# Performance work log

Hardware: AMD Instinct MI355X
Metric: run time of the kernel (lower is better)

The kernel has to match this reference:

```python
import jax, jax.numpy as jnp
import numpy as np

TEMP = 0.1
LAM = 1.0
NORM_EPS = 1e-12   # torch F.normalize eps
COS_EPS = 1e-8     # torch F.cosine_similarity eps


def l2norm(x, axis):
    n = jnp.sqrt(jnp.sum(x * x, axis=axis, keepdims=True))
    return x / jnp.maximum(n, NORM_EPS)


def cos_sim(a, b, axis):
    na = jnp.sqrt(jnp.sum(a * a, axis=axis))
    nb = jnp.sqrt(jnp.sum(b * b, axis=axis))
    return jnp.sum(a * b, axis=axis) / jnp.maximum(na * nb, COS_EPS)


def setup_inputs() -> dict:
    key = jax.random.key(0)
    k1, k2, k3, k4, k5 = jax.random.split(key, 5)
    B, C, H, W = 32, 256, 32, 32
    return {
        "q_b": jax.random.normal(k1, (B, C, H, W), dtype=jnp.float32),
        "k_b": jax.random.normal(k2, (B, C, H, W), dtype=jnp.float32),
        "q_grid": jax.random.normal(k3, (B, C, H, W), dtype=jnp.float32),
        "k_grid": jax.random.normal(k4, (B, C, H, W), dtype=jnp.float32),
        "labels": jax.random.randint(k5, (B,), 0, 10, dtype=jnp.int64),
    }


def densecl(q_b, k_b, q_grid, k_grid, labels):
    B, C, H, W = q_b.shape
    S = H * W
    q_b = l2norm(q_b, axis=1)
    k_b = l2norm(k_b, axis=1)
    q_grid = l2norm(q_grid, axis=1)
    k_grid = l2norm(k_grid, axis=1)

    q_b_flat = q_b.reshape(B, C, S)
    k_b_flat = k_b.reshape(B, C, S)
    # spatial correspondence: [B, S, S]
    sim = jnp.einsum('bci,bcj->bij', q_b_flat, k_b_flat)
    max_sim_idx = jnp.argmax(sim, axis=-1)  # [B, S]

    Cg = q_grid.shape[1]
    q_grid_flat = q_grid.reshape(B, Cg, S)
    k_grid_flat = k_grid.reshape(B, Cg, S)
    idx = jnp.broadcast_to(max_sim_idx[:, None, :], (B, Cg, S))
    k_matched = jnp.take_along_axis(k_grid_flat, idx, axis=2)
    pos_sim = cos_sim(q_grid_flat, k_matched, axis=1) / TEMP  # [B, S]

    # random negative from a different-label sample (use_prototypes=False path)
    key = jax.random.key(42)
    u = jax.random.uniform(key, (B, B))
    mask = labels[:, None] != labels[None, :]
    neg_idx = jnp.argmax(jnp.where(mask, u, -1.0), axis=1)  # [B]
    neg_k = k_grid_flat[neg_idx]  # [B, Cg, S]
    neg_sim = cos_sim(q_grid_flat, neg_k, axis=1) / TEMP  # [B, S]

    loss = -jnp.log(jnp.exp(pos_sim) / (jnp.exp(pos_sim) + jnp.exp(neg_sim) + 1e-6))
    return jnp.mean(loss)


def reference(q_b, k_b, q_grid, k_grid, labels):
    return densecl(q_b, k_b, q_grid, k_grid, labels) * LAM
```

## Files before the change

kernel.cpp:

```cpp
#include <hip/hip_runtime.h>
#include <hip/hip_bf16.h>
#include <math.h>
#include <stdint.h>

#define BB 32
#define CC 256
#define SS 1024

typedef __attribute__((ext_vector_type(8))) short short8v;
typedef __attribute__((ext_vector_type(4))) float f32x4;

#define ASYNC16(g, l)                                                        \
  __builtin_amdgcn_global_load_lds(                                          \
      (const __attribute__((address_space(1))) void*)(g),                    \
      (__attribute__((address_space(3))) void*)(l), 16, 0, 0)

__device__ __forceinline__ unsigned short bf16_rne(float f) {
  unsigned int u = __float_as_uint(f);
  unsigned int r = (u + 0x7fffu + ((u >> 16) & 1u)) >> 16;
  return (unsigned short)r;
}

__global__ __launch_bounds__(256, 4) void transnorm_kernel(
    const float* __restrict__ srcA, const float* __restrict__ srcB,
    unsigned short* __restrict__ dstA, unsigned short* __restrict__ dstB,
    float* __restrict__ invA, float* __restrict__ invB) {
  const int bid = blockIdx.x;
  const int which = bid >> 10;
  const int sub = bid & 1023;
  const int b = sub >> 5;
  const int s0 = (sub & 31) * 32;

  const float* src = which ? srcB : srcA;
  unsigned short* dst = which ? dstB : dstA;
  float* inv = which ? invB : invA;

  __shared__ float st[256][33];
  __shared__ float part[8][33];

  const int tid = threadIdx.x;
  const int s_l = tid & 31, c_off = tid >> 5;

  const float* sp = src + (size_t)b * CC * SS + s0 + s_l;
  float ssq = 0.f;
#pragma unroll 8
  for (int p = 0; p < 32; ++p) {
    int c = p * 8 + c_off;
    float x = sp[(size_t)c << 10];
    ssq = fmaf(x, x, ssq);
    st[c][s_l] = x;
  }
  part[c_off][s_l] = ssq;
  __syncthreads();

  const int chunk = tid >> 3, rb8 = tid & 7;
  unsigned short* dp = dst + ((size_t)b * SS + s0) * CC;
#pragma unroll
  for (int r0 = 0; r0 < 32; r0 += 8) {
    int r = r0 + rb8;
    unsigned short u[8];
#pragma unroll
    for (int uu = 0; uu < 8; ++uu) u[uu] = bf16_rne(st[chunk * 8 + uu][r]);
    uint4 pk;
    pk.x = (unsigned)u[0] | ((unsigned)u[1] << 16);
    pk.y = (unsigned)u[2] | ((unsigned)u[3] << 16);
    pk.z = (unsigned)u[4] | ((unsigned)u[5] << 16);
    pk.w = (unsigned)u[6] | ((unsigned)u[7] << 16);
    *(uint4*)(dp + (size_t)r * CC + chunk * 8) = pk;
  }
  if (inv != nullptr && tid < 32) {
    float s = 0.f;
#pragma unroll
    for (int k = 0; k < 8; ++k) s += part[k][tid];
    inv[b * SS + s0 + tid] = 1.0f / fmaxf(sqrtf(s), 1e-12f);
  }
}

__global__ __launch_bounds__(256, 4) void simargmax_mfma(
    const unsigned short* __restrict__ qt, const unsigned short* __restrict__ kt,
    const float* __restrict__ invk, unsigned long long* __restrict__ best) {
  const int i_raw = blockIdx.x;
  const int xcd = i_raw & 7;
  const int u = i_raw >> 3;
  const int b = ((u >> 6) << 3) | xcd;
  const int tile = u & 63;
  const int it = tile >> 3, jt = tile & 7;
  const int t = threadIdx.x, w = t >> 6, l = t & 63;

  __shared__ unsigned short sa[128 * 64];
  __shared__ unsigned short sb[128 * 64];
  __shared__ unsigned long long cand2[128][2];
  __shared__ float sinvk[128];

  if (t < 128) sinvk[t] = invk[b * SS + jt * 128 + t];

  const unsigned short* aG = qt + ((size_t)b * SS + it * 128) * CC;
  const unsigned short* bG = kt + ((size_t)b * SS + jt * 128) * CC;

  f32x4 acc[4][4];
#pragma unroll
  for (int mt = 0; mt < 4; ++mt)
#pragma unroll
    for (int nt = 0; nt < 4; ++nt) acc[mt][nt] = (f32x4){0.f, 0.f, 0.f, 0.f};

  const int r8 = l >> 3, p = l & 7;
  const int q4 = l >> 4, m16 = l & 15;
  const int wi = (w >> 1) * 64, wj = (w & 1) * 64;

  for (int ch = 0; ch < 4; ++ch) {
    __syncthreads();
#pragma unroll
    for (int v = 0; v < 4; ++v) {
      int r = v * 32 + w * 8 + r8;
      int clog = p ^ (r & 7);
      ASYNC16(aG + (size_t)r * CC + ch * 64 + clog * 8, &sa[(v * 32 + w * 8) * 64]);
      ASYNC16(bG + (size_t)r * CC + ch * 64 + clog * 8, &sb[(v * 32 + w * 8) * 64]);
    }
    __syncthreads();
#pragma unroll
    for (int kk = 0; kk < 2; ++kk) {
      short8v af[4], bf[4];
#pragma unroll
      for (int mt = 0; mt < 4; ++mt) {
        int i = wi + mt * 16 + m16;
        int cp = (kk * 4 + q4) ^ (i & 7);
        af[mt] = *(const short8v*)&sa[i * 64 + cp * 8];
        int j = wj + mt * 16 + m16;
        int cq = (kk * 4 + q4) ^ (j & 7);
        bf[mt] = *(const short8v*)&sb[j * 64 + cq * 8];
      }
#pragma unroll
      for (int mt = 0; mt < 4; ++mt)
#pragma unroll
        for (int nt = 0; nt < 4; ++nt)
          acc[mt][nt] = __builtin_amdgcn_mfma_f32_16x16x32_bf16(
              af[mt], bf[nt], acc[mt][nt], 0, 0, 0);
    }
  }

  float siv[4];
#pragma unroll
  for (int nt = 0; nt < 4; ++nt) siv[nt] = sinvk[wj + nt * 16 + m16];

#pragma unroll
  for (int mt = 0; mt < 4; ++mt) {
    unsigned long long bp[4];
#pragma unroll
    for (int e = 0; e < 4; ++e) {
      unsigned long long mx = 0ull;
#pragma unroll
      for (int nt = 0; nt < 4; ++nt) {
        float v = acc[mt][nt][e] * siv[nt];
        unsigned int uu = __float_as_uint(v);
        uu = (uu & 0x80000000u) ? ~uu : (uu | 0x80000000u);
        int col = jt * 128 + wj + nt * 16 + m16;
        unsigned long long pk =
            ((unsigned long long)uu << 32) | (unsigned)(1023 - col);
        mx = (pk > mx) ? pk : mx;
      }
      bp[e] = mx;
    }
#pragma unroll
    for (int d = 1; d < 16; d <<= 1) {
#pragma unroll
      for (int e = 0; e < 4; ++e) {
        unsigned long long o = __shfl_xor(bp[e], d, 64);
        if (o > bp[e]) bp[e] = o;
      }
    }
    if (m16 == 0) {
#pragma unroll
      for (int e = 0; e < 4; ++e)
        cand2[wi + mt * 16 + q4 * 4 + e][w & 1] = bp[e];
    }
  }
  __syncthreads();
  if (t < 128) {
    unsigned long long m0 = cand2[t][0], m1 = cand2[t][1];
    atomicMax(&best[b * SS + it * 128 + t], m0 > m1 ? m0 : m1);
  }
}

__device__ __forceinline__ void tf_round(uint32_t& x0, uint32_t& x1, int r) {
  x0 += x1;
  x1 = (x1 << r) | (x1 >> (32 - r));
  x1 ^= x0;
}

__global__ void negidx_kernel(const int* __restrict__ labels, int* __restrict__ negidx) {
  __shared__ float u[1024];
  int t = threadIdx.x;
  uint32_t x0 = (uint32_t)t;
  uint32_t x1 = (uint32_t)(t + 512);
  const uint32_t ks0 = 0u, ks1 = 42u, ks2 = 0x1BD11BDAu ^ 0u ^ 42u;
  x0 += ks0; x1 += ks1;
  tf_round(x0, x1, 13); tf_round(x0, x1, 15); tf_round(x0, x1, 26); tf_round(x0, x1, 6);
  x0 += ks1; x1 += ks2 + 1u;
  tf_round(x0, x1, 17); tf_round(x0, x1, 29); tf_round(x0, x1, 16); tf_round(x0, x1, 24);
  x0 += ks2; x1 += ks0 + 2u;
  tf_round(x0, x1, 13); tf_round(x0, x1, 15); tf_round(x0, x1, 26); tf_round(x0, x1, 6);
  x0 += ks0; x1 += ks1 + 3u;
  tf_round(x0, x1, 17); tf_round(x0, x1, 29); tf_round(x0, x1, 16); tf_round(x0, x1, 24);
  x0 += ks1; x1 += ks2 + 4u;
  tf_round(x0, x1, 13); tf_round(x0, x1, 15); tf_round(x0, x1, 26); tf_round(x0, x1, 6);
  x0 += ks2; x1 += ks0 + 5u;
  u[t]       = __uint_as_float((x0 >> 9) | 0x3f800000u) - 1.0f;
  u[t + 512] = __uint_as_float((x1 >> 9) | 0x3f800000u) - 1.0f;
  __syncthreads();
  if (t < BB) {
    int lb = labels[t];
    float bestv = -1.0f;
    int bj = 0;
    for (int j = 0; j < BB; ++j) {
      float v = (labels[j] != lb) ? u[t * BB + j] : -1.0f;
      if (v > bestv) { bestv = v; bj = j; }
    }
    negidx[t] = bj;
  }
}

__global__ __launch_bounds__(256) void loss_fused_kernel(
    const float* __restrict__ qg, const unsigned short* __restrict__ kgt,
    const float* __restrict__ invkg, const unsigned long long* __restrict__ best,
    const int* __restrict__ negidx, float* __restrict__ out) {
  const int tid = threadIdx.x;
  const int s_l = tid & 31, g = tid >> 5;
  const int P0 = blockIdx.x * 32;
  const int b = P0 >> 10;
  const int s = (P0 & (SS - 1)) + s_l;
  const int idx = b * SS + s;
  const int js = 1023 - (int)(best[idx] & 0xffffffffu);
  const int nb = negidx[b];

  const float* qcol = qg + ((size_t)b * CC + g * 32) * SS + s;
  const unsigned short* kp = kgt + ((size_t)b * SS + js) * CC + g * 32;
  const unsigned short* kn = kgt + ((size_t)nb * SS + s) * CC + g * 32;

  float dp = 0.f, dn = 0.f, sq = 0.f;
#pragma unroll
  for (int uu = 0; uu < 4; ++uu) {
    uint4 up = *(const uint4*)(kp + uu * 8);
    uint4 un = *(const uint4*)(kn + uu * 8);
    float q[8];
#pragma unroll
    for (int j = 0; j < 8; ++j) {
      q[j] = qcol[(size_t)(uu * 8 + j) << 10];
      sq = fmaf(q[j], q[j], sq);
    }
    float pv[8], nv[8];
    pv[0] = __uint_as_float(up.x << 16); pv[1] = __uint_as_float(up.x & 0xffff0000u);
    pv[2] = __uint_as_float(up.y << 16); pv[3] = __uint_as_float(up.y & 0xffff0000u);
    pv[4] = __uint_as_float(up.z << 16); pv[5] = __uint_as_float(up.z & 0xffff0000u);
    pv[6] = __uint_as_float(up.w << 16); pv[7] = __uint_as_float(up.w & 0xffff0000u);
    nv[0] = __uint_as_float(un.x << 16); nv[1] = __uint_as_float(un.x & 0xffff0000u);
    nv[2] = __uint_as_float(un.y << 16); nv[3] = __uint_as_float(un.y & 0xffff0000u);
    nv[4] = __uint_as_float(un.z << 16); nv[5] = __uint_as_float(un.z & 0xffff0000u);
    nv[6] = __uint_as_float(un.w << 16); nv[7] = __uint_as_float(un.w & 0xffff0000u);
#pragma unroll
    for (int j = 0; j < 8; ++j) {
      dp = fmaf(q[j], pv[j], dp);
      dn = fmaf(q[j], nv[j], dn);
    }
  }

  __shared__ float rdp[8][33], rdn[8][33], rsq[8][33];
  rdp[g][s_l] = dp;
  rdn[g][s_l] = dn;
  rsq[g][s_l] = sq;
  __syncthreads();
  if (tid < 32) {
    float DP = 0.f, DN = 0.f, SQ = 0.f;
#pragma unroll
    for (int k = 0; k < 8; ++k) {
      DP += rdp[k][tid];
      DN += rdn[k][tid];
      SQ += rsq[k][tid];
    }
    int s2 = (P0 & (SS - 1)) + tid;
    int idx2 = b * SS + s2;
    int js2 = 1023 - (int)(best[idx2] & 0xffffffffu);
    float iq = 1.0f / fmaxf(sqrtf(SQ), 1e-12f);
    float pvv = DP * iq * invkg[b * SS + js2] * 10.0f;
    float nvv = DN * iq * invkg[nb * SS + s2] * 10.0f;
    float elem = logf(expf(pvv) + expf(nvv) + 1e-6f) - pvv;
#pragma unroll
    for (int o = 16; o > 0; o >>= 1) elem += __shfl_down(elem, o, 32);
    if (tid == 0) atomicAdd(out, elem * (1.0f / (BB * SS)));
  }
}

__global__ __launch_bounds__(256) void norms_kernel(
    const float* __restrict__ qb, const float* __restrict__ kb,
    const float* __restrict__ qg, const float* __restrict__ kg,
    float* __restrict__ inv) {
  int t = blockIdx.x * 256 + threadIdx.x;
  int which = t >> 15;
  int bs = t & (BB * SS - 1);
  const float* src = (which == 0) ? qb : (which == 1) ? kb : (which == 2) ? qg : kg;
  int b = bs >> 10;
  int s = bs & (SS - 1);
  const float* p = src + (size_t)b * CC * SS + s;
  float ss = 0.f;
#pragma unroll 8
  for (int c = 0; c < CC; ++c) {
    float x = p[(size_t)c * SS];
    ss = fmaf(x, x, ss);
  }
  float n = fmaxf(sqrtf(ss), 1e-12f);
  inv[t] = 1.0f / n;
}

#define TI 64
#define TJ 128
#define KC 32

__global__ __launch_bounds__(256) void simargmax_kernel(
    const float* __restrict__ qb, const float* __restrict__ kb,
    const float* __restrict__ invq, const float* __restrict__ invk,
    int* __restrict__ amax) {
  const int b = blockIdx.x >> 4;
  const int i0 = (blockIdx.x & 15) * TI;
  const int t = threadIdx.x;
  const int ti = t >> 4;
  const int tj = t & 15;

  __shared__ float aQ[KC][TI];
  __shared__ float bK[KC][TJ];
  __shared__ float redv[TI][16];
  __shared__ int redj[TI][16];

  const float* qbase = qb + (size_t)b * CC * SS + i0;
  const float* kbase = kb + (size_t)b * CC * SS;
  const float* ivq = invq + b * SS + i0;
  const float* ivk = invk + b * SS;

  float best_v = -3.4e38f;
  int best_j = 0;

  for (int j0 = 0; j0 < SS; j0 += TJ) {
    float acc[4][8];
#pragma unroll
    for (int r = 0; r < 4; ++r)
#pragma unroll
      for (int rr = 0; rr < 8; ++rr) acc[r][rr] = 0.f;

    for (int c0 = 0; c0 < CC; c0 += KC) {
      __syncthreads();
#pragma unroll
      for (int v = 0; v < 2; ++v) {
        int f = t + v * 256;
        int cl = f >> 4;
        int sl = (f & 15) << 2;
        float4 qa = *(const float4*)(qbase + (size_t)(c0 + cl) * SS + sl);
        float4 iv = *(const float4*)(ivq + sl);
        aQ[cl][sl + 0] = qa.x * iv.x;
        aQ[cl][sl + 1] = qa.y * iv.y;
        aQ[cl][sl + 2] = qa.z * iv.z;
        aQ[cl][sl + 3] = qa.w * iv.w;
      }
#pragma unroll
      for (int v = 0; v < 4; ++v) {
        int f = t + v * 256;
        int cl = f >> 5;
        int sl = (f & 31) << 2;
        float4 ka = *(const float4*)(kbase + (size_t)(c0 + cl) * SS + j0 + sl);
        float4 ik = *(const float4*)(ivk + j0 + sl);
        bK[cl][sl + 0] = ka.x * ik.x;
        bK[cl][sl + 1] = ka.y * ik.y;
        bK[cl][sl + 2] = ka.z * ik.z;
        bK[cl][sl + 3] = ka.w * ik.w;
      }
      __syncthreads();
#pragma unroll
      for (int kc = 0; kc < KC; ++kc) {
        float4 a0 = *(const float4*)&aQ[kc][ti * 4];
        float4 b0 = *(const float4*)&bK[kc][tj * 8];
        float4 b1 = *(const float4*)&bK[kc][tj * 8 + 4];
        float av[4] = {a0.x, a0.y, a0.z, a0.w};
        float bv[8] = {b0.x, b0.y, b0.z, b0.w, b1.x, b1.y, b1.z, b1.w};
#pragma unroll
        for (int r = 0; r < 4; ++r)
#pragma unroll
          for (int rr = 0; rr < 8; ++rr)
            acc[r][rr] = fmaf(av[r], bv[rr], acc[r][rr]);
      }
    }
    __syncthreads();
#pragma unroll
    for (int r = 0; r < 4; ++r) {
      float v = acc[r][0];
      int jb = j0 + tj * 8;
#pragma unroll
      for (int rr = 1; rr < 8; ++rr) {
        if (acc[r][rr] > v) { v = acc[r][rr]; jb = j0 + tj * 8 + rr; }
      }
      redv[ti * 4 + r][tj] = v;
      redj[ti * 4 + r][tj] = jb;
    }
    __syncthreads();
    if (t < TI) {
#pragma unroll
      for (int ww = 0; ww < 16; ++ww) {
        float v = redv[t][ww];
        if (v > best_v) { best_v = v; best_j = redj[t][ww]; }
      }
    }
  }
  if (t < TI) amax[b * SS + i0 + t] = best_j;
}

__global__ __launch_bounds__(256) void loss_kernel(
    const float* __restrict__ qg, const float* __restrict__ kg,
    const float* __restrict__ invq, const float* __restrict__ invk,
    const int* __restrict__ amax, const int* __restrict__ negidx,
    float* __restrict__ out) {
  int t = blockIdx.x * 256 + threadIdx.x;
  int b = t >> 10;
  int s = t & (SS - 1);
  int js = amax[t];
  int nb = negidx[b];
  const float* qcol = qg + (size_t)b * CC * SS + s;
  const float* kpcol = kg + (size_t)b * CC * SS + js;
  const float* kncol = kg + (size_t)nb * CC * SS + s;
  float dp = 0.f, dn = 0.f;
#pragma unroll 8
  for (int c = 0; c < CC; ++c) {
    float q = qcol[(size_t)c * SS];
    dp = fmaf(q, kpcol[(size_t)c * SS], dp);
    dn = fmaf(q, kncol[(size_t)c * SS], dn);
  }
  float iq = invq[t];
  float pv = dp * iq * invk[b * SS + js] * 10.0f;
  float nv = dn * iq * invk[nb * SS + s] * 10.0f;
  float elem = logf(expf(pv) + expf(nv) + 1e-6f) - pv;

  __shared__ float red[256];
  red[threadIdx.x] = elem;
  __syncthreads();
  for (int o = 128; o > 0; o >>= 1) {
    if (threadIdx.x < o) red[threadIdx.x] += red[threadIdx.x + o];
    __syncthreads();
  }
  if (threadIdx.x == 0) atomicAdd(out, red[0] * (1.0f / (BB * SS)));
}

extern "C" void kernel_launch(void* const* d_in, const int* in_sizes, int n_in,
                              void* d_out, int out_size, void* d_ws, size_t ws_size,
                              hipStream_t stream) {
  const float* qb = (const float*)d_in[0];
  const float* kb = (const float*)d_in[1];
  const float* qg = (const float*)d_in[2];
  const float* kg = (const float*)d_in[3];
  const int* labels = (const int*)d_in[4];

  char* ws = (char*)d_ws;
  float* invkb = (float*)ws;
  float* invkg = (float*)(ws + 128 * 1024);
  unsigned long long* best = (unsigned long long*)(ws + 256 * 1024);
  int* negidx = (int*)(ws + 512 * 1024);
  unsigned short* qt = (unsigned short*)(ws + (1 << 20));
  unsigned short* kt = (unsigned short*)(ws + (17 << 20));
  unsigned short* kgt = (unsigned short*)(ws + (33 << 20));

  const size_t need = (size_t)50 * 1024 * 1024;
  const bool fast = ws_size >= need;

  hipMemsetAsync(d_out, 0, sizeof(float), stream);

  if (fast) {
    hipMemsetAsync(best, 0, BB * SS * sizeof(unsigned long long), stream);
    negidx_kernel<<<1, 512, 0, stream>>>(labels, negidx);
    transnorm_kernel<<<2048, 256, 0, stream>>>(qb, kb, qt, kt, nullptr, invkb);
    simargmax_mfma<<<2048, 256, 0, stream>>>(qt, kt, invkb, best);
    transnorm_kernel<<<1024, 256, 0, stream>>>(kg, kg, kgt, kgt, invkg, invkg);
    loss_fused_kernel<<<1024, 256, 0, stream>>>(qg, kgt, invkg, best, negidx,
                                                (float*)d_out);
  } else {
    float* inv = (float*)ws;
    int* amax = (int*)(ws + 512 * 1024);
    int* negidx2 = (int*)(ws + 640 * 1024);
    norms_kernel<<<(4 * BB * SS) / 256, 256, 0, stream>>>(qb, kb, qg, kg, inv);
    simargmax_kernel<<<BB * (SS / TI), 256, 0, stream>>>(
        qb, kb, inv + 0 * BB * SS, inv + 1 * BB * SS, amax);
    negidx_kernel<<<1, 512, 0, stream>>>(labels, negidx2);
    loss_kernel<<<(BB * SS) / 256, 256, 0, stream>>>(
        qg, kg, inv + 2 * BB * SS, inv + 3 * BB * SS, amax, negidx2,
        (float*)d_out);
  }
}
```

Measured before the change: 226.6 us.

## Fuse bf16 conversion and key norm into similarity argmax kernel

The separate transpose/normalize pass over q_b and k_b is removed. The MFMA similarity kernel now reads fp32 inputs directly, converts them to bf16 in shared memory, and accumulates the key norms itself. This drops a kernel launch and the bf16 intermediate round-trip through memory. In exchange, each tile rereads fp32 data several times across blocks, stages loads through registers instead of async LDS loads, and repeats the conversion work.

Result: slower. 295.4 us (+30.4%).

```diff
diff --git a/kernel.cpp b/kernel.cpp
--- a/kernel.cpp
+++ b/kernel.cpp
@@ -10,15 +10,148 @@
 typedef __attribute__((ext_vector_type(8))) short short8v;
 typedef __attribute__((ext_vector_type(4))) float f32x4;
 
-#define ASYNC16(g, l)                                                        \
-  __builtin_amdgcn_global_load_lds(                                          \
-      (const __attribute__((address_space(1))) void*)(g),                    \
-      (__attribute__((address_space(3))) void*)(l), 16, 0, 0)
-
 __device__ __forceinline__ unsigned short bf16_rne(float f) {
   unsigned int u = __float_as_uint(f);
   unsigned int r = (u + 0x7fffu + ((u >> 16) & 1u)) >> 16;
   return (unsigned short)r;
+}
+
+__global__ __launch_bounds__(256, 4) void simargmax_fused(
+    const float* __restrict__ qb, const float* __restrict__ kb,
+    unsigned long long* __restrict__ best) {
+  const int i_raw = blockIdx.x;
+  const int xcd = i_raw & 7;
+  const int u = i_raw >> 3;
+  const int b = ((u >> 6) << 3) | xcd;
+  const int tile = u & 63;
+  const int it = tile >> 3, jt = tile & 7;
+  const int t = threadIdx.x, w = t >> 6, l = t & 63;
+
+  __shared__ unsigned short sa[128 * 64];
+  __shared__ unsigned short sb[128 * 64];
+  __shared__ unsigned long long cand2[128][2];
+  __shared__ float nrm[128][2];
+  __shared__ float sinvk[128];
+
+  const float* aG = qb + (size_t)b * CC * SS + it * 128;
+  const float* bG = kb + (size_t)b * CC * SS + jt * 128;
+
+  const int srow = t & 127, chalf = t >> 7;
+
+  f32x4 acc[4][4];
+#pragma unroll
+  for (int mt = 0; mt < 4; ++mt)
+#pragma unroll
+    for (int nt = 0; nt < 4; ++nt) acc[mt][nt] = (f32x4){0.f, 0.f, 0.f, 0.f};
+
+  const int q4 = l >> 4, m16 = l & 15;
+  const int wi = (w >> 1) * 64, wj = (w & 1) * 64;
+
+  float nsq = 0.f;
+
+  for (int ch = 0; ch < 4; ++ch) {
+    float ra[32], rb_[32];
+    const float* pa = aG + (size_t)(ch * 64 + chalf * 32) * SS + srow;
+    const float* pb = bG + (size_t)(ch * 64 + chalf * 32) * SS + srow;
+#pragma unroll
+    for (int j = 0; j < 32; ++j) ra[j] = pa[(size_t)j * SS];
+#pragma unroll
+    for (int j = 0; j < 32; ++j) rb_[j] = pb[(size_t)j * SS];
+
+    __syncthreads();
+
+#pragma unroll
+    for (int m = 0; m < 4; ++m) {
+      short8v pk;
+#pragma unroll
+      for (int k = 0; k < 8; ++k) pk[k] = (short)bf16_rne(ra[m * 8 + k]);
+      int clog = chalf * 4 + m;
+      int phys = clog ^ (srow & 7);
+      *(short8v*)&sa[srow * 64 + phys * 8] = pk;
+    }
+#pragma unroll
+    for (int m = 0; m < 4; ++m) {
+      short8v pk;
+#pragma unroll
+      for (int k = 0; k < 8; ++k) {
+        float x = rb_[m * 8 + k];
+        nsq = fmaf(x, x, nsq);
+        pk[k] = (short)bf16_rne(x);
+      }
+      int clog = chalf * 4 + m;
+      int phys = clog ^ (srow & 7);
+      *(short8v*)&sb[srow * 64 + phys * 8] = pk;
+    }
+    __syncthreads();
+
+#pragma unroll
+    for (int kk = 0; kk < 2; ++kk) {
+      short8v af[4], bf[4];
+#pragma unroll
+      for (int mt = 0; mt < 4; ++mt) {
+        int i = wi + mt * 16 + m16;
+        int cp = (kk * 4 + q4) ^ (i & 7);
+        af[mt] = *(const short8v*)&sa[i * 64 + cp * 8];
+        int j = wj + mt * 16 + m16;
+        int cq = (kk * 4 + q4) ^ (j & 7);
+        bf[mt] = *(const short8v*)&sb[j * 64 + cq * 8];
+      }
+#pragma unroll
+      for (int mt = 0; mt < 4; ++mt)
+#pragma unroll
+        for (int nt = 0; nt < 4; ++nt)
+          acc[mt][nt] = __builtin_amdgcn_mfma_f32_16x16x32_bf16(
+              af[mt], bf[nt], acc[mt][nt], 0, 0, 0);
+    }
+  }
+
+  nrm[srow][chalf] = nsq;
+  __syncthreads();
+  if (t < 128)
+    sinvk[t] = 1.0f / fmaxf(sqrtf(nrm[t][0] + nrm[t][1]), 1e-12f);
+  __syncthreads();
+
+  float siv[4];
+#pragma unroll
+  for (int nt = 0; nt < 4; ++nt) siv[nt] = sinvk[wj + nt * 16 + m16];
+
+#pragma unroll
+  for (int mt = 0; mt < 4; ++mt) {
+    unsigned long long bp[4];
+#pragma unroll
+    for (int e = 0; e < 4; ++e) {
+      unsigned long long mx = 0ull;
+#pragma unroll
+      for (int nt = 0; nt < 4; ++nt) {
+        float v = acc[mt][nt][e] * siv[nt];
+        unsigned int uu = __float_as_uint(v);
+        uu = (uu & 0x80000000u) ? ~uu : (uu | 0x80000000u);
+        int col = jt * 128 + wj + nt * 16 + m16;
+        unsigned long long pk =
+            ((unsigned long long)uu << 32) | (unsigned)(1023 - col);
+        mx = (pk > mx) ? pk : mx;
+      }
+      bp[e] = mx;
+    }
+#pragma unroll
+    for (int d = 1; d < 16; d <<= 1) {
+#pragma unroll
+      for (int e = 0; e < 4; ++e) {
+        unsigned long long o = __shfl_xor(bp[e], d, 64);
+        if (o > bp[e]) bp[e] = o;
+      }
+    }
+    if (m16 == 0) {
+#pragma unroll
+      for (int e = 0; e < 4; ++e)
+        cand2[wi + mt * 16 + q4 * 4 + e][w & 1] = bp[e];
+    }
+  }
+  __syncthreads();
+  if (t < 128) {
+    unsigned long long m0 = cand2[t][0], m1 = cand2[t][1];
+    atomicMax(&best[b * SS + it * 128 + t], m0 > m1 ? m0 : m1);
+  }
 }
 
 __global__ __launch_bounds__(256, 4) void transnorm_kernel(
@@ -73,111 +206,6 @@
 #pragma unroll
     for (int k = 0; k < 8; ++k) s += part[k][tid];
     inv[b * SS + s0 + tid] = 1.0f / fmaxf(sqrtf(s), 1e-12f);
-  }
-}
-
-__global__ __launch_bounds__(256, 4) void simargmax_mfma(
-    const unsigned short* __restrict__ qt, const unsigned short* __restrict__ kt,
-    const float* __restrict__ invk, unsigned long long* __restrict__ best) {
-  const int i_raw = blockIdx.x;
-  const int xcd = i_raw & 7;
-  const int u = i_raw >> 3;
-  const int b = ((u >> 6) << 3) | xcd;
-  const int tile = u & 63;
-  const int it = tile >> 3, jt = tile & 7;
-  const int t = threadIdx.x, w = t >> 6, l = t & 63;
-
-  __shared__ unsigned short sa[128 * 64];
-  __shared__ unsigned short sb[128 * 64];
-  __shared__ unsigned long long cand2[128][2];
-  __shared__ float sinvk[128];
-
-  if (t < 128) sinvk[t] = invk[b * SS + jt * 128 + t];
-
-  const unsigned short* aG = qt + ((size_t)b * SS + it * 128) * CC;
-  const unsigned short* bG = kt + ((size_t)b * SS + jt * 128) * CC;
-
-  f32x4 acc[4][4];
-#pragma unroll
-  for (int mt = 0; mt < 4; ++mt)
-#pragma unroll
-    for (int nt = 0; nt < 4; ++nt) acc[mt][nt] = (f32x4){0.f, 0.f, 0.f, 0.f};
-
-  const int r8 = l >> 3, p = l & 7;
-  const int q4 = l >> 4, m16 = l & 15;
-  const int wi = (w >> 1) * 64, wj = (w & 1) * 64;
-
-  for (int ch = 0; ch < 4; ++ch) {
-    __syncthreads();
-#pragma unroll
-    for (int v = 0; v < 4; ++v) {
-      int r = v * 32 + w * 8 + r8;
-      int clog = p ^ (r & 7);
-      ASYNC16(aG + (size_t)r * CC + ch * 64 + clog * 8, &sa[(v * 32 + w * 8) * 64]);
-      ASYNC16(bG + (size_t)r * CC + ch * 64 + clog * 8, &sb[(v * 32 + w * 8) * 64]);
-    }
-    __syncthreads();
-#pragma unroll
-    for (int kk = 0; kk < 2; ++kk) {
-      short8v af[4], bf[4];
-#pragma unroll
-      for (int mt = 0; mt < 4; ++mt) {
-        int i = wi + mt * 16 + m16;
-        int cp = (kk * 4 + q4) ^ (i & 7);
-        af[mt] = *(const short8v*)&sa[i * 64 + cp * 8];
-        int j = wj + mt * 16 + m16;
-        int cq = (kk * 4 + q4) ^ (j & 7);
-        bf[mt] = *(const short8v*)&sb[j * 64 + cq * 8];
-      }
-#pragma unroll
-      for (int mt = 0; mt < 4; ++mt)
-#pragma unroll
-        for (int nt = 0; nt < 4; ++nt)
-          acc[mt][nt] = __builtin_amdgcn_mfma_f32_16x16x32_bf16(
-              af[mt], bf[nt], acc[mt][nt], 0, 0, 0);
-    }
-  }
-
-  float siv[4];
-#pragma unroll
-  for (int nt = 0; nt < 4; ++nt) siv[nt] = sinvk[wj + nt * 16 + m16];
-
-#pragma unroll
-  for (int mt = 0; mt < 4; ++mt) {
-    unsigned long long bp[4];
-#pragma unroll
-    for (int e = 0; e < 4; ++e) {
-      unsigned long long mx = 0ull;
-#pragma unroll
-      for (int nt = 0; nt < 4; ++nt) {
-        float v = acc[mt][nt][e] * siv[nt];
-        unsigned int uu = __float_as_uint(v);
-        uu = (uu & 0x80000000u) ? ~uu : (uu | 0x80000000u);
-        int col = jt * 128 + wj + nt * 16 + m16;
-        unsigned long long pk =
-            ((unsigned long long)uu << 32) | (unsigned)(1023 - col);
-        mx = (pk > mx) ? pk : mx;
-      }
-      bp[e] = mx;
-    }
-#pragma unroll
-    for (int d = 1; d < 16; d <<= 1) {
-#pragma unroll
-      for (int e = 0; e < 4; ++e) {
-        unsigned long long o = __shfl_xor(bp[e], d, 64);
-        if (o > bp[e]) bp[e] = o;
-      }
-    }
-    if (m16 == 0) {
-#pragma unroll
-      for (int e = 0; e < 4; ++e)
-        cand2[wi + mt * 16 + q4 * 4 + e][w & 1] = bp[e];
-    }
-  }
-  __syncthreads();
-  if (t < 128) {
-    unsigned long long m0 = cand2[t][0], m1 = cand2[t][1];
-    atomicMax(&best[b * SS + it * 128 + t], m0 > m1 ? m0 : m1);
   }
 }
 
@@ -454,15 +482,12 @@
   const int* labels = (const int*)d_in[4];
 
   char* ws = (char*)d_ws;
-  float* invkb = (float*)ws;
-  float* invkg = (float*)(ws + 128 * 1024);
+  float* invkg = (float*)ws;
   unsigned long long* best = (unsigned long long*)(ws + 256 * 1024);
   int* negidx = (int*)(ws + 512 * 1024);
-  unsigned short* qt = (unsigned short*)(ws + (1 << 20));
-  unsigned short* kt = (unsigned short*)(ws + (17 << 20));
-  unsigned short* kgt = (unsigned short*)(ws + (33 << 20));
-
-  const size_t need = (size_t)50 * 1024 * 1024;
+  unsigned short* kgt = (unsigned short*)(ws + (1 << 20));
+
+  const size_t need = (size_t)18 * 1024 * 1024;
   const bool fast = ws_size >= need;
 
   hipMemsetAsync(d_out, 0, sizeof(float), stream);
@@ -470,8 +495,7 @@
   if (fast) {
     hipMemsetAsync(best, 0, BB * SS * sizeof(unsigned long long), stream);
     negidx_kernel<<<1, 512, 0, stream>>>(labels, negidx);
-    transnorm_kernel<<<2048, 256, 0, stream>>>(qb, kb, qt, kt, nullptr, invkb);
-    simargmax_mfma<<<2048, 256, 0, stream>>>(qt, kt, invkb, best);
+    simargmax_fused<<<2048, 256, 0, stream>>>(qb, kb, best);
     transnorm_kernel<<<1024, 256, 0, stream>>>(kg, kg, kgt, kgt, invkg, invkg);
     loss_fused_kernel<<<1024, 256, 0, stream>>>(qg, kgt, invkg, best, negidx,
                                                 (float*)d_out);
```
